# Optimization experiments

Measured on AMD Instinct MI355X. Metric: run time of the kernel, lower is better.

## Reference

```python
import jax, jax.numpy as jnp
import numpy as np

N = 50000      # nodes
E = 800000     # edges
IN = 128       # in_dim
EMB = 32       # emb_dim
ED = 8         # edge_dim
L = 4          # num_layers
B = 64         # num graphs in batch
OUT = 10       # out_dim
EPS = 1e-5


def setup_inputs() -> dict:
    key = jax.random.key(0)
    ks = jax.random.split(key, 16)
    f32 = jnp.float32
    def nrm(k, shape, scale):
        return jax.random.normal(k, shape, dtype=f32) * scale
    inp = {}
    inp['x'] = nrm(ks[0], (N, IN), 1.0)
    inp['edge_index'] = jax.random.randint(ks[1], (2, E), 0, N)
    inp['edge_attr'] = nrm(ks[2], (E, ED), 1.0)
    inp['batch'] = jnp.sort(jax.random.randint(ks[3], (N,), 0, B))
    # lin_in
    inp['lin_in_w'] = nrm(ks[4], (IN, EMB), 0.05)
    inp['lin_in_b'] = jnp.zeros((EMB,), f32)
    # per-layer message MLP: Linear(2e+ed->e), BN, ReLU, Linear(e->e), BN, ReLU
    inp['msg_w1'] = nrm(ks[5], (L, 2 * EMB + ED, EMB), 0.1)
    inp['msg_b1'] = jnp.zeros((L, EMB), f32)
    inp['msg_g1'] = jnp.ones((L, EMB), f32)
    inp['msg_be1'] = jnp.zeros((L, EMB), f32)
    inp['msg_w2'] = nrm(ks[6], (L, EMB, EMB), 0.1)
    inp['msg_b2'] = jnp.zeros((L, EMB), f32)
    inp['msg_g2'] = jnp.ones((L, EMB), f32)
    inp['msg_be2'] = jnp.zeros((L, EMB), f32)
    # per-layer update MLP: Linear(2e->e), BN, ReLU, Linear(e->e), BN, ReLU
    inp['upd_w1'] = nrm(ks[7], (L, 2 * EMB, EMB), 0.1)
    inp['upd_b1'] = jnp.zeros((L, EMB), f32)
    inp['upd_g1'] = jnp.ones((L, EMB), f32)
    inp['upd_be1'] = jnp.zeros((L, EMB), f32)
    inp['upd_w2'] = nrm(ks[8], (L, EMB, EMB), 0.1)
    inp['upd_b2'] = jnp.zeros((L, EMB), f32)
    inp['upd_g2'] = jnp.ones((L, EMB), f32)
    inp['upd_be2'] = jnp.zeros((L, EMB), f32)
    # lin_pred
    inp['pred_w'] = nrm(ks[9], (EMB, OUT), 0.1)
    inp['pred_b'] = jnp.zeros((OUT,), f32)
    return inp


def _bn(x, g, b):
    # BatchNorm1d in training mode: batch stats over dim 0 (biased variance)
    mu = jnp.mean(x, axis=0)
    var = jnp.mean(jnp.square(x - mu), axis=0)
    return (x - mu) * jax.lax.rsqrt(var + EPS) * g + b


def reference(x, edge_attr, lin_in_w, lin_in_b,
              msg_w1, msg_b1, msg_g1, msg_be1, msg_w2, msg_b2, msg_g2, msg_be2,
              upd_w1, upd_b1, upd_g1, upd_be1, upd_w2, upd_b2, upd_g2, upd_be2,
              pred_w, pred_b, edge_index, batch):
    src = edge_index[0]  # h_j source nodes
    dst = edge_index[1]  # h_i target nodes (aggregation index)
    h = x @ lin_in_w + lin_in_b  # [N, EMB]
    for i in range(L):
        # message: gather + concat + MLP(BN,ReLU)x2 over edges
        msg_in = jnp.concatenate([h[dst], h[src], edge_attr], axis=-1)  # [E, 2e+ed]
        m = jax.nn.relu(_bn(msg_in @ msg_w1[i] + msg_b1[i], msg_g1[i], msg_be1[i]))
        m = jax.nn.relu(_bn(m @ msg_w2[i] + msg_b2[i], msg_g2[i], msg_be2[i]))
        # aggregate: scatter-add by destination
        aggr = jax.ops.segment_sum(m, dst, num_segments=N)  # [N, EMB]
        # update: concat + MLP(BN,ReLU)x2
        u = jnp.concatenate([h, aggr], axis=-1)  # [N, 2e]
        u = jax.nn.relu(_bn(u @ upd_w1[i] + upd_b1[i], upd_g1[i], upd_be1[i]))
        u = jax.nn.relu(_bn(u @ upd_w2[i] + upd_b2[i], upd_g2[i], upd_be2[i]))
        h = u + h  # residual in MPNNModel.get_embeddings
    # global mean pool
    sums = jax.ops.segment_sum(h, batch, num_segments=B)
    counts = jax.ops.segment_sum(jnp.ones((N,), h.dtype), batch, num_segments=B)
    h_graph = sums / jnp.maximum(counts, 1.0)[:, None]
    return h_graph @ pred_w + pred_b  # [B, OUT]
```

## Files before the change

kernel.cpp:

```cpp
#include <hip/hip_runtime.h>
#include <cstddef>

#define N_NODES 50000
#define N_EDGES 800000
#define IN_DIM  128
#define EMB     32
#define ED      8
#define NLAYERS 4
#define NB      64
#define OUTD    10
#define EPS_BN  1e-5f

#define EDGE_GRID 3125
#define NODE_GRID 196
#define NODE4_GRID 782
#define AU_GRID   6250
#define MSG1_EPT  2
#define MSG1_GRID 1563
#define NT16      50000
#define NTILE_N   3125
#define LIN_GRID  782
#define MSG2_TPW  16
#define MSG2_GRID 782

#define SREP 4

typedef short bf16x8 __attribute__((ext_vector_type(8)));
typedef float f32x4  __attribute__((ext_vector_type(4)));


__device__ __forceinline__ unsigned short f2bf(float x) {
  union { float f; unsigned u; } v; v.f = x;
  unsigned b = v.u + 0x7FFFu + ((v.u >> 16) & 1u);
  return (unsigned short)(b >> 16);
}
__device__ __forceinline__ float bf2f(unsigned short s) {
  union { unsigned u; float f; } v; v.u = ((unsigned)s) << 16;
  return v.f;
}

__device__ __forceinline__ void coef_from_stats(const float* __restrict__ stats_stage,
                                                const float* __restrict__ g,
                                                const float* __restrict__ be,
                                                float inv_count, float* __restrict__ cf) {
  if (threadIdx.x < EMB) {
    const int c = threadIdx.x;
    float s = 0.f, ss = 0.f;
#pragma unroll
    for (int r = 0; r < SREP; ++r) {
      s  += stats_stage[r*64 + c];
      ss += stats_stage[r*64 + EMB + c];
    }
    const float mu  = s * inv_count;
    const float var = ss * inv_count - mu*mu;
    const float a = g[c] * rsqrtf(var + EPS_BN);
    cf[c] = a;
    cf[EMB + c] = fmaf(-mu, a, be[c]);
  }
  __syncthreads();
}

__device__ __forceinline__ void block_stats_atomic(const float ts[EMB], const float tss[EMB],
                                                   float* __restrict__ stats_stage) {
  __shared__ float sred[256];
  const int lane = threadIdx.x & 63;
  const int wid  = threadIdx.x >> 6;
#pragma unroll
  for (int c = 0; c < EMB; ++c) {
    float a = ts[c];
    float q = tss[c];
#pragma unroll
    for (int o = 32; o > 0; o >>= 1) {
      a += __shfl_down(a, o, 64);
      q += __shfl_down(q, o, 64);
    }
    if (lane == 0) { sred[wid*64 + c] = a; sred[wid*64 + EMB + c] = q; }
  }
  __syncthreads();
  if (threadIdx.x < 64) {
    const float v = sred[threadIdx.x] + sred[64 + threadIdx.x] +
                    sred[128 + threadIdx.x] + sred[192 + threadIdx.x];
    atomicAdd(stats_stage + ((blockIdx.x & (SREP-1)) << 6) + threadIdx.x, v);
  }
}

__device__ __forceinline__ void wave_stats_atomic(float ts[8], float tss[8],
                                                  float* __restrict__ lds_s,
                                                  float* __restrict__ lds_q,
                                                  float* __restrict__ stats_stage) {
  const int lane = threadIdx.x & 63;
  const int wv   = threadIdx.x >> 6;
#pragma unroll
  for (int j = 0; j < 8; ++j) {
    float a = ts[j], b = tss[j];
#pragma unroll
    for (int o = 32; o > 0; o >>= 1) {
      a += __shfl_down(a, o, 64);
      b += __shfl_down(b, o, 64);
    }
    ts[j] = a; tss[j] = b;
  }
  if (lane == 0) {
#pragma unroll
    for (int j = 0; j < 8; ++j) {
      lds_s[wv*8 + j] = ts[j];
      lds_q[wv*8 + j] = tss[j];
    }
  }
  __syncthreads();
  if (threadIdx.x < 64) {
    const float v = (threadIdx.x < 32) ? lds_s[threadIdx.x] : lds_q[threadIdx.x - 32];
    atomicAdd(stats_stage + ((blockIdx.x & (SREP-1)) << 6) + threadIdx.x, v);
  }
}

#define HSTRIDE 40

__global__ __launch_bounds__(256) void k_lin_in_pq(
    const float* __restrict__ x, const float* __restrict__ w, const float* __restrict__ b,
    const float* __restrict__ w1, const float* __restrict__ b1, const int* __restrict__ ei,
    float* __restrict__ h, unsigned short* __restrict__ p, unsigned short* __restrict__ q,
    int* __restrict__ cnt)
{
  __shared__ __align__(16) unsigned short lds_hb[4][16*HSTRIDE];
  __shared__ __align__(16) unsigned short lds_pq[4][16*HSTRIDE];
  const int lane = threadIdx.x & 63;
  const int wv   = threadIdx.x >> 6;
  const int n0i  = lane & 15;
  const int quad = lane >> 4;

  const int tile = blockIdx.x*4 + wv;
  if (tile < NTILE_N) {
    const int r0 = tile*16;
    bf16x8 BwL[4], BwH[4];
#pragma unroll
    for (int kb = 0; kb < 4; ++kb) {
#pragma unroll
      for (int j = 0; j < 8; ++j) {
        const int k = kb*32 + quad*8 + j;
        BwL[kb][j] = (short)f2bf(w[k*EMB + n0i]);
        BwH[kb][j] = (short)f2bf(w[k*EMB + 16 + n0i]);
      }
    }
    f32x4 accL = {0.f,0.f,0.f,0.f};
    f32x4 accH = {0.f,0.f,0.f,0.f};
#pragma unroll
    for (int kb = 0; kb < 4; ++kb) {
      const float4 xa = *(const float4*)(x + (size_t)(r0 + n0i)*IN_DIM + kb*32 + quad*8);
      const float4 xb = *(const float4*)(x + (size_t)(r0 + n0i)*IN_DIM + kb*32 + quad*8 + 4);
      bf16x8 A;
      A[0] = (short)f2bf(xa.x); A[1] = (short)f2bf(xa.y);
      A[2] = (short)f2bf(xa.z); A[3] = (short)f2bf(xa.w);
      A[4] = (short)f2bf(xb.x); A[5] = (short)f2bf(xb.y);
      A[6] = (short)f2bf(xb.z); A[7] = (short)f2bf(xb.w);
      accL = __builtin_amdgcn_mfma_f32_16x16x32_bf16(A, BwL[kb], accL, 0, 0, 0);
      accH = __builtin_amdgcn_mfma_f32_16x16x32_bf16(A, BwH[kb], accH, 0, 0, 0);
    }
    const float bL = b[n0i], bH = b[16 + n0i];
#pragma unroll
    for (int r = 0; r < 4; ++r) {
      const int row = quad*4 + r;
      const float vL = accL[r] + bL;
      const float vH = accH[r] + bH;
      h[(size_t)(r0 + row)*EMB + n0i]      = vL;
      h[(size_t)(r0 + row)*EMB + 16 + n0i] = vH;
      lds_hb[wv][row*HSTRIDE + n0i]      = f2bf(vL);
      lds_hb[wv][row*HSTRIDE + 16 + n0i] = f2bf(vH);
    }
    bf16x8 A2;
#pragma unroll
    for (int j = 0; j < 8; ++j)
      A2[j] = (short)lds_hb[wv][n0i*HSTRIDE + quad*8 + j];
    bf16x8 BpL, BpH, BqL, BqH;
#pragma unroll
    for (int j = 0; j < 8; ++j) {
      const int k = quad*8 + j;
      BpL[j] = (short)f2bf(w1[k*EMB + n0i]);
      BpH[j] = (short)f2bf(w1[k*EMB + 16 + n0i]);
      BqL[j] = (short)f2bf(w1[(EMB + k)*EMB + n0i]);
      BqH[j] = (short)f2bf(w1[(EMB + k)*EMB + 16 + n0i]);
    }
    const f32x4 z4 = {0.f,0.f,0.f,0.f};
    f32x4 pL = __builtin_amdgcn_mfma_f32_16x16x32_bf16(A2, BpL, z4, 0, 0, 0);
    f32x4 pH = __builtin_amdgcn_mfma_f32_16x16x32_bf16(A2, BpH, z4, 0, 0, 0);
    f32x4 qL = __builtin_amdgcn_mfma_f32_16x16x32_bf16(A2, BqL, z4, 0, 0, 0);
    f32x4 qH = __builtin_amdgcn_mfma_f32_16x16x32_bf16(A2, BqH, z4, 0, 0, 0);
    const float b1L = b1[n0i], b1H = b1[16 + n0i];
#pragma unroll
    for (int r = 0; r < 4; ++r) {
      const int row = quad*4 + r;
      lds_pq[wv][row*HSTRIDE + n0i]      = f2bf(pL[r] + b1L);
      lds_pq[wv][row*HSTRIDE + 16 + n0i] = f2bf(pH[r] + b1H);
    }
    {
      const int row2 = lane >> 2;
      const int c8   = (lane & 3)*8;
      const uint4 ov = *(const uint4*)&lds_pq[wv][row2*HSTRIDE + c8];
      *(uint4*)(p + (size_t)(r0 + row2)*EMB + c8) = ov;
    }
#pragma unroll
    for (int r = 0; r < 4; ++r) {
      const int row = quad*4 + r;
      lds_pq[wv][row*HSTRIDE + n0i]      = f2bf(qL[r]);
      lds_pq[wv][row*HSTRIDE + 16 + n0i] = f2bf(qH[r]);
    }
    {
      const int row2 = lane >> 2;
      const int c8   = (lane & 3)*8;
      const uint4 ov = *(const uint4*)&lds_pq[wv][row2*HSTRIDE + c8];
      *(uint4*)(q + (size_t)(r0 + row2)*EMB + c8) = ov;
    }
  }
  for (int e = blockIdx.x*256 + threadIdx.x; e < N_EDGES; e += gridDim.x*256)
    atomicAdd(&cnt[ei[N_EDGES + e]], 1);
}

__global__ __launch_bounds__(256) void k_scan_a(const int* __restrict__ cnt,
                                                int* __restrict__ row_ptr, int* __restrict__ bsum) {
  __shared__ int s[256];
  const int gid = blockIdx.x*256 + threadIdx.x;
  const int v = (gid < N_NODES) ? cnt[gid] : 0;
  s[threadIdx.x] = v;
  __syncthreads();
  for (int o = 1; o < 256; o <<= 1) {
    const int t = (threadIdx.x >= o) ? s[threadIdx.x - o] : 0;
    __syncthreads();
    s[threadIdx.x] += t;
    __syncthreads();
  }
  if (gid < N_NODES) row_ptr[gid] = s[threadIdx.x] - v;
  if (threadIdx.x == 255) bsum[blockIdx.x] = s[255];
}

__global__ __launch_bounds__(256) void k_scan_bc(int* __restrict__ row_ptr,
                                                 const int* __restrict__ bsum) {
  __shared__ int s[256];
  const int t = threadIdx.x;
  const int v = (t < NODE_GRID) ? bsum[t] : 0;
  s[t] = v;
  __syncthreads();
  for (int o = 1; o < 256; o <<= 1) {
    const int tt = (t >= o) ? s[t - o] : 0;
    __syncthreads();
    s[t] += tt;
    __syncthreads();
  }
  const int off = (blockIdx.x == 0) ? 0 : s[blockIdx.x - 1];
  const int gid = blockIdx.x*256 + t;
  if (gid < N_NODES) row_ptr[gid] += off;
  if (blockIdx.x == 0 && t == 0) row_ptr[N_NODES] = N_EDGES;
}

__global__ __launch_bounds__(256) void k_place(const int* __restrict__ ei,
                                               const int* __restrict__ row_ptr,
                                               int* __restrict__ cnt2, int* __restrict__ perm) {
  const int e = blockIdx.x*256 + threadIdx.x;
  const int d = ei[N_EDGES + e];
  const int pos = row_ptr[d] + atomicAdd(&cnt2[d], 1);
  perm[pos] = e;
}

__global__ __launch_bounds__(256) void k_permute(
    const int* __restrict__ perm, const int* __restrict__ ei, const float* __restrict__ ea,
    int* __restrict__ src_perm, int* __restrict__ dst_perm, unsigned short* __restrict__ ea_perm)
{
  const int i = blockIdx.x*256 + threadIdx.x;
  const int e = perm[i];
  src_perm[i] = ei[e];
  dst_perm[i] = ei[N_EDGES + e];
  const float4 v0 = ((const float4*)(ea + (size_t)e*ED))[0];
  const float4 v1 = ((const float4*)(ea + (size_t)e*ED))[1];
  const float ev[8] = {v0.x, v0.y, v0.z, v0.w, v1.x, v1.y, v1.z, v1.w};
  unsigned u[4];
#pragma unroll
  for (int j = 0; j < 4; ++j)
    u[j] = (unsigned)f2bf(ev[2*j]) | ((unsigned)f2bf(ev[2*j+1]) << 16);
  uint4 o; o.x = u[0]; o.y = u[1]; o.z = u[2]; o.w = u[3];
  *(uint4*)(ea_perm + (size_t)i*ED) = o;
}


__global__ __launch_bounds__(256) void k_msg1(
    const unsigned short* __restrict__ pb, const unsigned short* __restrict__ qb,
    const int* __restrict__ src_perm, const int* __restrict__ dst_perm,
    const unsigned short* __restrict__ ea_perm,
    const float* __restrict__ w1b,
    unsigned short* __restrict__ y, float* __restrict__ stats)
{
  float ts[EMB], tss[EMB];
#pragma unroll
  for (int c = 0; c < EMB; ++c) { ts[c] = 0.f; tss[c] = 0.f; }
  const int base = blockIdx.x*(256*MSG1_EPT) + threadIdx.x;
  for (int it = 0; it < MSG1_EPT; ++it) {
    const int i = base + it*256;
    if (i >= N_EDGES) break;
    const int dst = dst_perm[i];
    const int src = src_perm[i];
    float acc[EMB];
    const uint4* pd = (const uint4*)(pb + (size_t)dst*EMB);
    const uint4* qs = (const uint4*)(qb + (size_t)src*EMB);
#pragma unroll
    for (int j4 = 0; j4 < 4; ++j4) {
      const uint4 a = pd[j4];
      const uint4 b = qs[j4];
      const unsigned ua[4] = {a.x, a.y, a.z, a.w};
      const unsigned ub[4] = {b.x, b.y, b.z, b.w};
#pragma unroll
      for (int t = 0; t < 4; ++t) {
        acc[j4*8 + 2*t]   = bf2f((unsigned short)(ua[t] & 0xFFFFu)) +
                            bf2f((unsigned short)(ub[t] & 0xFFFFu));
        acc[j4*8 + 2*t+1] = bf2f((unsigned short)(ua[t] >> 16)) +
                            bf2f((unsigned short)(ub[t] >> 16));
      }
    }
    const uint4 eraw = *(const uint4*)(ea_perm + (size_t)i*ED);
    const unsigned ue[4] = {eraw.x, eraw.y, eraw.z, eraw.w};
    float ev[8];
#pragma unroll
    for (int t = 0; t < 4; ++t) {
      ev[2*t]   = bf2f((unsigned short)(ue[t] & 0xFFFFu));
      ev[2*t+1] = bf2f((unsigned short)(ue[t] >> 16));
    }
#pragma unroll
    for (int k = 0; k < 8; ++k) {
      const float* wk = w1b + k*EMB;
#pragma unroll
      for (int c = 0; c < EMB; ++c) acc[c] = fmaf(ev[k], wk[c], acc[c]);
    }
    unsigned short us[EMB];
#pragma unroll
    for (int c = 0; c < EMB; ++c) us[c] = f2bf(acc[c]);
    unsigned u[16];
#pragma unroll
    for (int j = 0; j < 16; ++j)
      u[j] = (unsigned)us[2*j] | ((unsigned)us[2*j+1] << 16);
    uint4* dp = (uint4*)(y + (size_t)i*EMB);
#pragma unroll
    for (int j = 0; j < 4; ++j) {
      uint4 o; o.x = u[4*j]; o.y = u[4*j+1]; o.z = u[4*j+2]; o.w = u[4*j+3];
      dp[j] = o;
    }
#pragma unroll
    for (int c = 0; c < EMB; ++c) {
      const float v = bf2f(us[c]);
      ts[c] += v;
      tss[c] = fmaf(v, v, tss[c]);
    }
  }
  block_stats_atomic(ts, tss, stats);
}

__global__ __launch_bounds__(256) void k_msg2(
    unsigned short* __restrict__ y,
    const float* __restrict__ stats1, const float* __restrict__ g1, const float* __restrict__ be1,
    const float* __restrict__ w2, const float* __restrict__ b2,
    float* __restrict__ stats2)
{
  __shared__ __align__(16) unsigned short lds_t[4][16*32];
  __shared__ float lds_s[4][32], lds_q[4][32];
  __shared__ float cf[64];

  coef_from_stats(stats1, g1, be1, 1.0f/(float)N_EDGES, cf);

  const int lane = threadIdx.x & 63;
  const int wid  = threadIdx.x >> 6;
  const int n0 = lane & 15;
  const int kb = lane >> 4;

  bf16x8 Blo, Bhi;
#pragma unroll
  for (int j = 0; j < 8; ++j) {
    Blo[j] = (short)f2bf(w2[(kb*8 + j)*EMB + n0]);
    Bhi[j] = (short)f2bf(w2[(kb*8 + j)*EMB + 16 + n0]);
  }
  float a1[8], c1[8];
#pragma unroll
  for (int j = 0; j < 8; ++j) {
    a1[j] = cf[kb*8 + j];
    c1[j] = cf[EMB + kb*8 + j];
  }
  const float b2c0 = b2[n0], b2c1 = b2[16 + n0];

  float ts[8], tss[8];
#pragma unroll
  for (int j = 0; j < 8; ++j) { ts[j] = 0.f; tss[j] = 0.f; }

  const int tile0 = blockIdx.x * (MSG2_TPW*4);
  for (int t = 0; t < MSG2_TPW; ++t) {
    const int tile = tile0 + t*4 + wid;
    if (tile >= NT16) break;
    const size_t e0 = (size_t)tile * 16;

    const uint4 araw = *(const uint4*)(y + (e0 + n0)*EMB + kb*8);
    unsigned int ua[4] = {araw.x, araw.y, araw.z, araw.w};
    bf16x8 A;
#pragma unroll
    for (int j = 0; j < 4; ++j) {
      float v0 = bf2f((unsigned short)(ua[j] & 0xFFFFu));
      float v1 = bf2f((unsigned short)(ua[j] >> 16));
      v0 = fmaxf(fmaf(a1[2*j],   v0, c1[2*j]),   0.f);
      v1 = fmaxf(fmaf(a1[2*j+1], v1, c1[2*j+1]), 0.f);
      A[2*j]   = (short)f2bf(v0);
      A[2*j+1] = (short)f2bf(v1);
    }

    f32x4 acc0 = {0.f, 0.f, 0.f, 0.f};
    f32x4 acc1 = {0.f, 0.f, 0.f, 0.f};
    acc0 = __builtin_amdgcn_mfma_f32_16x16x32_bf16(A, Blo, acc0, 0, 0, 0);
    acc1 = __builtin_amdgcn_mfma_f32_16x16x32_bf16(A, Bhi, acc1, 0, 0, 0);

#pragma unroll
    for (int r = 0; r < 4; ++r) {
      const int row = kb*4 + r;
      lds_t[wid][row*32 + n0]      = f2bf(acc0[r] + b2c0);
      lds_t[wid][row*32 + 16 + n0] = f2bf(acc1[r] + b2c1);
    }
    const uint4 orow = *(const uint4*)&lds_t[wid][(lane>>2)*32 + (lane&3)*8];
    *(uint4*)(y + (e0 + (lane>>2))*EMB + (lane&3)*8) = orow;

    unsigned int uo[4] = {orow.x, orow.y, orow.z, orow.w};
#pragma unroll
    for (int j = 0; j < 4; ++j) {
      const float v0 = bf2f((unsigned short)(uo[j] & 0xFFFFu));
      const float v1 = bf2f((unsigned short)(uo[j] >> 16));
      ts[2*j]   += v0;  tss[2*j]   = fmaf(v0, v0, tss[2*j]);
      ts[2*j+1] += v1;  tss[2*j+1] = fmaf(v1, v1, tss[2*j+1]);
    }
  }

#pragma unroll
  for (int j = 0; j < 8; ++j) {
    float s = ts[j], qq = tss[j];
#pragma unroll
    for (int o = 4; o < 64; o <<= 1) {
      s  += __shfl_xor(s, o, 64);
      qq += __shfl_xor(qq, o, 64);
    }
    ts[j] = s; tss[j] = qq;
  }
  if (lane < 4) {
#pragma unroll
    for (int j = 0; j < 8; ++j) {
      lds_s[wid][lane*8 + j] = ts[j];
      lds_q[wid][lane*8 + j] = tss[j];
    }
  }
  __syncthreads();
  if (threadIdx.x < 64) {
    const int c = threadIdx.x & 31;
    const int kind = threadIdx.x >> 5;
    float v = 0.f;
#pragma unroll
    for (int wq = 0; wq < 4; ++wq)
      v += kind ? lds_q[wq][c] : lds_s[wq][c];
    atomicAdd(stats2 + ((blockIdx.x & (SREP-1)) << 6) + kind*32 + c, v);
  }
}

__global__ __launch_bounds__(256) void k_aggr_upd1(
    const unsigned short* __restrict__ y, const int* __restrict__ row_ptr,
    const float* __restrict__ h,
    const float* __restrict__ stats1, const float* __restrict__ g2, const float* __restrict__ be2,
    const float* __restrict__ uw1, const float* __restrict__ ub1,
    float* __restrict__ z, float* __restrict__ stats2)
{
  __shared__ float cf[64];
  __shared__ float lh[8][32];
  __shared__ float la[8][32];
  __shared__ float rs[4][32], rq[4][32];
  coef_from_stats(stats1, g2, be2, 1.0f/(float)N_EDGES, cf);

  const int g = threadIdx.x >> 5;
  const int l = threadIdx.x & 31;
  const int n = blockIdx.x*8 + g;

  lh[g][l] = h[(size_t)n*EMB + l];

  const int rof = l >> 4;
  const int cp  = l & 15;
  const float a0 = cf[2*cp],     b0 = cf[EMB + 2*cp];
  const float a1 = cf[2*cp + 1], b1 = cf[EMB + 2*cp + 1];
  const int lo = row_ptr[n], hi = row_ptr[n+1];
  float s0 = 0.f, s1 = 0.f;
  for (int i = lo + rof; i < hi; i += 2) {
    const unsigned u = *(const unsigned*)(y + (size_t)i*EMB + 2*cp);
    const float v0 = bf2f((unsigned short)(u & 0xFFFFu));
    const float v1 = bf2f((unsigned short)(u >> 16));
    s0 += fmaxf(fmaf(a0, v0, b0), 0.f);
    s1 += fmaxf(fmaf(a1, v1, b1), 0.f);
  }
  s0 += __shfl_xor(s0, 16, 64);
  s1 += __shfl_xor(s1, 16, 64);
  if (rof == 0) { la[g][2*cp] = s0; la[g][2*cp + 1] = s1; }
  __syncthreads();

  float acc = ub1[l];
#pragma unroll
  for (int k = 0; k < EMB; ++k) acc = fmaf(lh[g][k], uw1[k*EMB + l], acc);
#pragma unroll
  for (int k = 0; k < EMB; ++k) acc = fmaf(la[g][k], uw1[(EMB + k)*EMB + l], acc);
  z[(size_t)n*EMB + l] = acc;

  const float sq = acc*acc;
  const float a2 = acc + __shfl_down(acc, 32, 64);
  const float q2 = sq  + __shfl_down(sq,  32, 64);
  const int wv = threadIdx.x >> 6;
  if ((threadIdx.x & 63) < 32) { rs[wv][l] = a2; rq[wv][l] = q2; }
  __syncthreads();
  if (threadIdx.x < 64) {
    const int c = threadIdx.x & 31;
    const int kind = threadIdx.x >> 5;
    float v = 0.f;
#pragma unroll
    for (int wq = 0; wq < 4; ++wq)
      v += kind ? rq[wq][c] : rs[wq][c];
    atomicAdd(stats2 + ((blockIdx.x & (SREP-1)) << 6) + kind*32 + c, v);
  }
}

__global__ __launch_bounds__(256) void k_upd2(
    float* __restrict__ z,
    const float* __restrict__ stats1, const float* __restrict__ g1, const float* __restrict__ be1,
    const float* __restrict__ w, const float* __restrict__ b,
    float* __restrict__ stats2)
{
  __shared__ float cf[64];
  __shared__ float lds_s[32], lds_q[32];
  coef_from_stats(stats1, g1, be1, 1.0f/(float)N_NODES, cf);

  const int lane = threadIdx.x & 63;
  const int wv   = threadIdx.x >> 6;
  const int n  = blockIdx.x*64 + lane;
  const int c0 = wv*8;
  float acc[8];
#pragma unroll
  for (int j = 0; j < 8; ++j) acc[j] = 0.f;
  if (n < N_NODES) {
#pragma unroll
    for (int j = 0; j < 8; ++j) acc[j] = b[c0 + j];
    const float4* zp = (const float4*)(z + (size_t)n*EMB);
#pragma unroll
    for (int k4 = 0; k4 < 8; ++k4) {
      const float4 v = zp[k4];
      const float mv[4] = {v.x, v.y, v.z, v.w};
#pragma unroll
      for (int t = 0; t < 4; ++t) {
        const int k = 4*k4 + t;
        const float m = fmaxf(fmaf(cf[k], mv[t], cf[EMB + k]), 0.f);
        const float* wk = w + k*EMB + c0;
#pragma unroll
        for (int j = 0; j < 8; ++j) acc[j] = fmaf(m, wk[j], acc[j]);
      }
    }
  }
  float ts[8], tss[8];
#pragma unroll
  for (int j = 0; j < 8; ++j) { ts[j] = acc[j]; tss[j] = acc[j]*acc[j]; }
  wave_stats_atomic(ts, tss, lds_s, lds_q, stats2);
  if (n < N_NODES) {
    float4 o0, o1;
    o0.x = acc[0]; o0.y = acc[1]; o0.z = acc[2]; o0.w = acc[3];
    o1.x = acc[4]; o1.y = acc[5]; o1.z = acc[6]; o1.w = acc[7];
    *(float4*)(z + (size_t)n*EMB + c0)     = o0;
    *(float4*)(z + (size_t)n*EMB + c0 + 4) = o1;
  }
}

__global__ __launch_bounds__(256) void k_resid_pq(
    float* __restrict__ h, const float* __restrict__ z,
    const float* __restrict__ stats, const float* __restrict__ g, const float* __restrict__ be,
    const float* __restrict__ w1_next, const float* __restrict__ b1_next,
    unsigned short* __restrict__ p, unsigned short* __restrict__ q)
{
  __shared__ float cf[64];
  __shared__ float lds_h[64][33];
  coef_from_stats(stats, g, be, 1.0f/(float)N_NODES, cf);

  const int lane = threadIdx.x & 63;
  const int wv   = threadIdx.x >> 6;
  const int n  = blockIdx.x*64 + lane;
  const int c0 = wv*8;
  if (n < N_NODES) {
    const float4* zp = (const float4*)(z + (size_t)n*EMB + c0);
    float4* hp = (float4*)(h + (size_t)n*EMB + c0);
    float hn[8];
    const float4 z0 = zp[0], z1 = zp[1];
    const float4 h0 = hp[0], h1 = hp[1];
    const float zv[8] = {z0.x, z0.y, z0.z, z0.w, z1.x, z1.y, z1.z, z1.w};
    const float hv[8] = {h0.x, h0.y, h0.z, h0.w, h1.x, h1.y, h1.z, h1.w};
#pragma unroll
    for (int j = 0; j < 8; ++j) {
      const int k = c0 + j;
      hn[j] = hv[j] + fmaxf(fmaf(cf[k], zv[j], cf[EMB + k]), 0.f);
      lds_h[lane][k] = hn[j];
    }
    float4 o0, o1;
    o0.x = hn[0]; o0.y = hn[1]; o0.z = hn[2]; o0.w = hn[3];
    o1.x = hn[4]; o1.y = hn[5]; o1.z = hn[6]; o1.w = hn[7];
    hp[0] = o0; hp[1] = o1;
  }
  __syncthreads();
  if (n < N_NODES && w1_next) {
    float ap[8], aq[8];
#pragma unroll
    for (int j = 0; j < 8; ++j) { ap[j] = b1_next[c0 + j]; aq[j] = 0.f; }
#pragma unroll
    for (int k = 0; k < EMB; ++k) {
      const float hvv = lds_h[lane][k];
      const float* wp = w1_next + k*EMB + c0;
      const float* wq = w1_next + (EMB + k)*EMB + c0;
#pragma unroll
      for (int j = 0; j < 8; ++j) ap[j] = fmaf(hvv, wp[j], ap[j]);
#pragma unroll
      for (int j = 0; j < 8; ++j) aq[j] = fmaf(hvv, wq[j], aq[j]);
    }
    unsigned up[4], uq[4];
#pragma unroll
    for (int j = 0; j < 4; ++j) {
      up[j] = (unsigned)f2bf(ap[2*j]) | ((unsigned)f2bf(ap[2*j+1]) << 16);
      uq[j] = (unsigned)f2bf(aq[2*j]) | ((unsigned)f2bf(aq[2*j+1]) << 16);
    }
    uint4 op; op.x = up[0]; op.y = up[1]; op.z = up[2]; op.w = up[3];
    uint4 oq; oq.x = uq[0]; oq.y = uq[1]; oq.z = uq[2]; oq.w = uq[3];
    *(uint4*)(p + (size_t)n*EMB + c0) = op;
    *(uint4*)(q + (size_t)n*EMB + c0) = oq;
  }
}

__global__ void k_pool(const float* __restrict__ h, const int* __restrict__ batch,
                       const float* __restrict__ pw, const float* __restrict__ pb,
                       float* __restrict__ out)
{
  __shared__ float sred[256];
  __shared__ float hg[EMB];
  const int b = blockIdx.x;
  int lo = 0, hi = N_NODES;
  while (lo < hi) { int m = (lo + hi) >> 1; if (batch[m] < b) lo = m + 1; else hi = m; }
  const int start = lo;
  hi = N_NODES;
  while (lo < hi) { int m = (lo + hi) >> 1; if (batch[m] < b + 1) lo = m + 1; else hi = m; }
  const int end = lo;

  const int c = threadIdx.x & (EMB-1);
  const int r = threadIdx.x >> 5;
  float s = 0.f;
  for (int n = start + r; n < end; n += 8) s += h[(size_t)n*EMB + c];
  sred[threadIdx.x] = s;
  __syncthreads();
  if (threadIdx.x < EMB) {
    float tot = 0.f;
#pragma unroll
    for (int r2 = 0; r2 < 8; ++r2) tot += sred[r2*EMB + threadIdx.x];
    const float cnt = (float)(end - start);
    hg[threadIdx.x] = tot / fmaxf(cnt, 1.f);
  }
  __syncthreads();
  if (threadIdx.x < OUTD) {
    float acc = pb[threadIdx.x];
#pragma unroll
    for (int cc = 0; cc < EMB; ++cc) acc = fmaf(hg[cc], pw[cc*OUTD + threadIdx.x], acc);
    out[b*OUTD + threadIdx.x] = acc;
  }
}


extern "C" void kernel_launch(void* const* d_in, const int* in_sizes, int n_in,
                              void* d_out, int out_size, void* d_ws, size_t ws_size,
                              hipStream_t stream) {
  const float* x        = (const float*)d_in[0];
  const int*   ei       = (const int*)  d_in[1];
  const float* ea       = (const float*)d_in[2];
  const int*   batch    = (const int*)  d_in[3];
  const float* lin_in_w = (const float*)d_in[4];
  const float* lin_in_b = (const float*)d_in[5];
  const float* msg_w1   = (const float*)d_in[6];
  const float* msg_b1   = (const float*)d_in[7];
  const float* msg_g1   = (const float*)d_in[8];
  const float* msg_be1  = (const float*)d_in[9];
  const float* msg_w2   = (const float*)d_in[10];
  const float* msg_b2   = (const float*)d_in[11];
  const float* msg_g2   = (const float*)d_in[12];
  const float* msg_be2  = (const float*)d_in[13];
  const float* upd_w1   = (const float*)d_in[14];
  const float* upd_b1   = (const float*)d_in[15];
  const float* upd_g1   = (const float*)d_in[16];
  const float* upd_be1  = (const float*)d_in[17];
  const float* upd_w2   = (const float*)d_in[18];
  const float* upd_b2   = (const float*)d_in[19];
  const float* upd_g2   = (const float*)d_in[20];
  const float* upd_be2  = (const float*)d_in[21];
  const float* pred_w   = (const float*)d_in[22];
  const float* pred_b   = (const float*)d_in[23];
  float* out = (float*)d_out;

  char* wsb = (char*)d_ws;
  unsigned short* y  = (unsigned short*)wsb;
  unsigned short* eap= (unsigned short*)(wsb + (size_t)N_EDGES*EMB*2);
  unsigned short* p  = eap + (size_t)N_EDGES*ED;
  unsigned short* q  = p + (size_t)N_NODES*EMB;
  float* h       = (float*)(q + (size_t)N_NODES*EMB);
  float* z       = h + (size_t)N_NODES*EMB;
  float* stats   = z + (size_t)N_NODES*EMB;
  int*   cnt     = (int*)(stats + 16*SREP*64);
  int*   cnt2    = cnt + N_NODES;
  int*   row_ptr = cnt2 + N_NODES;
  int*   bsum    = row_ptr + N_NODES + 1;
  int*   perm    = bsum + 256;
  int*   src_perm= perm + N_EDGES;
  int*   dst_perm= src_perm + N_EDGES;
  const size_t need = ((size_t)((char*)(dst_perm + N_EDGES) - wsb));
  if (ws_size < need) return;

  hipMemsetAsync(stats, 0, (16*SREP*64 + 2*N_NODES)*sizeof(float), stream);

  k_lin_in_pq<<<LIN_GRID, 256, 0, stream>>>(x, lin_in_w, lin_in_b, msg_w1, msg_b1, ei,
                                            h, p, q, cnt);
  k_scan_a<<<NODE_GRID, 256, 0, stream>>>(cnt, row_ptr, bsum);
  k_scan_bc<<<NODE_GRID, 256, 0, stream>>>(row_ptr, bsum);
  k_place<<<EDGE_GRID, 256, 0, stream>>>(ei, row_ptr, cnt2, perm);
  k_permute<<<EDGE_GRID, 256, 0, stream>>>(perm, ei, ea, src_perm, dst_perm, eap);

  for (int l = 0; l < NLAYERS; ++l) {
    const int st = l*4;
    const float* w1  = msg_w1 + (size_t)l*(2*EMB+ED)*EMB;
    const float* w1b = w1 + (size_t)2*EMB*EMB;
    const float* w2  = msg_w2 + (size_t)l*EMB*EMB;
    const float* uw1 = upd_w1 + (size_t)l*(2*EMB)*EMB;
    const float* uw2 = upd_w2 + (size_t)l*EMB*EMB;
    const float* w1_next = (l+1 < NLAYERS) ? msg_w1 + (size_t)(l+1)*(2*EMB+ED)*EMB : nullptr;
    const float* b1_next = (l+1 < NLAYERS) ? msg_b1 + (size_t)(l+1)*EMB : nullptr;

    k_msg1<<<MSG1_GRID, 256, 0, stream>>>(p, q, src_perm, dst_perm, eap,
                                          w1b, y, stats + (size_t)st*SREP*64);
    k_msg2<<<MSG2_GRID, 256, 0, stream>>>(y, stats + (size_t)st*SREP*64,
                                          msg_g1 + l*EMB, msg_be1 + l*EMB,
                                          w2, msg_b2 + l*EMB, stats + (size_t)(st+1)*SREP*64);
    k_aggr_upd1<<<AU_GRID, 256, 0, stream>>>(y, row_ptr, h,
                                             stats + (size_t)(st+1)*SREP*64,
                                             msg_g2 + l*EMB, msg_be2 + l*EMB,
                                             uw1, upd_b1 + l*EMB,
                                             z, stats + (size_t)(st+2)*SREP*64);
    k_upd2<<<NODE4_GRID, 256, 0, stream>>>(z, stats + (size_t)(st+2)*SREP*64,
                                           upd_g1 + l*EMB, upd_be1 + l*EMB,
                                           uw2, upd_b2 + l*EMB, stats + (size_t)(st+3)*SREP*64);
    k_resid_pq<<<NODE4_GRID, 256, 0, stream>>>(h, z, stats + (size_t)(st+3)*SREP*64,
                                               upd_g2 + l*EMB, upd_be2 + l*EMB,
                                               w1_next, b1_next, p, q);
  }

  k_pool<<<NB, 256, 0, stream>>>(h, batch, pred_w, pred_b, out);
}
```

Measured before the change: 904.3 us.

## Recompute first message linear layer instead of storing intermediate edge activations

The first message kernel now only accumulates BatchNorm statistics and no longer writes the per-edge pre-BN activations. A fused kernel recomputes the gather plus edge-attr linear layer, applies BN1 and ReLU, runs the second linear layer on MFMA through LDS, and writes the output and its statistics. This drops one full E×32 bf16 write and one read per layer, paid for by a second round of gathers from p/q and repeated edge-attr FMAs. Stats are now taken from fp32 values rather than bf16-rounded ones, a small numerical change.

```diff
diff --git a/kernel.cpp b/kernel.cpp
--- a/kernel.cpp
+++ b/kernel.cpp
@@ -17,12 +17,11 @@
 #define AU_GRID   6250
 #define MSG1_EPT  2
 #define MSG1_GRID 1563
-#define NT16      50000
+#define NCHUNK    12500
+#define MSG12_CPW 4
+#define MSG12_GRID 782
 #define NTILE_N   3125
 #define LIN_GRID  782
-#define MSG2_TPW  16
-#define MSG2_GRID 782
-
 #define SREP 4
 
 typedef short bf16x8 __attribute__((ext_vector_type(8)));
@@ -111,6 +110,42 @@
   if (threadIdx.x < 64) {
     const float v = (threadIdx.x < 32) ? lds_s[threadIdx.x] : lds_q[threadIdx.x - 32];
     atomicAdd(stats_stage + ((blockIdx.x & (SREP-1)) << 6) + threadIdx.x, v);
+  }
+}
+
+__device__ __forceinline__ void y1_compute(float acc[EMB],
+    const unsigned short* __restrict__ pb, const unsigned short* __restrict__ qb,
+    int dst, int src, const unsigned short* __restrict__ ea_perm, int i,
+    const float* __restrict__ w1b) {
+  const uint4* pd = (const uint4*)(pb + (size_t)dst*EMB);
+  const uint4* qs = (const uint4*)(qb + (size_t)src*EMB);
+#pragma unroll
+  for (int j4 = 0; j4 < 4; ++j4) {
+    const uint4 a = pd[j4];
+    const uint4 b = qs[j4];
+    const unsigned ua[4] = {a.x, a.y, a.z, a.w};
+    const unsigned ub[4] = {b.x, b.y, b.z, b.w};
+#pragma unroll
+    for (int t = 0; t < 4; ++t) {
+      acc[j4*8 + 2*t]   = bf2f((unsigned short)(ua[t] & 0xFFFFu)) +
+                          bf2f((unsigned short)(ub[t] & 0xFFFFu));
+      acc[j4*8 + 2*t+1] = bf2f((unsigned short)(ua[t] >> 16)) +
+                          bf2f((unsigned short)(ub[t] >> 16));
+    }
+  }
+  const uint4 eraw = *(const uint4*)(ea_perm + (size_t)i*ED);
+  const unsigned ue[4] = {eraw.x, eraw.y, eraw.z, eraw.w};
+  float ev[8];
+#pragma unroll
+  for (int t = 0; t < 4; ++t) {
+    ev[2*t]   = bf2f((unsigned short)(ue[t] & 0xFFFFu));
+    ev[2*t+1] = bf2f((unsigned short)(ue[t] >> 16));
+  }
+#pragma unroll
+  for (int k = 0; k < 8; ++k) {
+    const float* wk = w1b + k*EMB;
+#pragma unroll
+    for (int c = 0; c < EMB; ++c) acc[c] = fmaf(ev[k], wk[c], acc[c]);
   }
 }
 
@@ -280,12 +315,11 @@
 }
 
 
-__global__ __launch_bounds__(256) void k_msg1(
+__global__ __launch_bounds__(256) void k_msg1_stats(
     const unsigned short* __restrict__ pb, const unsigned short* __restrict__ qb,
     const int* __restrict__ src_perm, const int* __restrict__ dst_perm,
     const unsigned short* __restrict__ ea_perm,
-    const float* __restrict__ w1b,
-    unsigned short* __restrict__ y, float* __restrict__ stats)
+    const float* __restrict__ w1b, float* __restrict__ stats)
 {
   float ts[EMB], tss[EMB];
 #pragma unroll
@@ -294,137 +328,113 @@
   for (int it = 0; it < MSG1_EPT; ++it) {
     const int i = base + it*256;
     if (i >= N_EDGES) break;
-    const int dst = dst_perm[i];
-    const int src = src_perm[i];
     float acc[EMB];
-    const uint4* pd = (const uint4*)(pb + (size_t)dst*EMB);
-    const uint4* qs = (const uint4*)(qb + (size_t)src*EMB);
-#pragma unroll
-    for (int j4 = 0; j4 < 4; ++j4) {
-      const uint4 a = pd[j4];
-      const uint4 b = qs[j4];
-      const unsigned ua[4] = {a.x, a.y, a.z, a.w};
-      const unsigned ub[4] = {b.x, b.y, b.z, b.w};
-#pragma unroll
-      for (int t = 0; t < 4; ++t) {
-        acc[j4*8 + 2*t]   = bf2f((unsigned short)(ua[t] & 0xFFFFu)) +
-                            bf2f((unsigned short)(ub[t] & 0xFFFFu));
-        acc[j4*8 + 2*t+1] = bf2f((unsigned short)(ua[t] >> 16)) +
-                            bf2f((unsigned short)(ub[t] >> 16));
-      }
-    }
-    const uint4 eraw = *(const uint4*)(ea_perm + (size_t)i*ED);
-    const unsigned ue[4] = {eraw.x, eraw.y, eraw.z, eraw.w};
-    float ev[8];
-#pragma unroll
-    for (int t = 0; t < 4; ++t) {
-      ev[2*t]   = bf2f((unsigned short)(ue[t] & 0xFFFFu));
-      ev[2*t+1] = bf2f((unsigned short)(ue[t] >> 16));
-    }
-#pragma unroll
-    for (int k = 0; k < 8; ++k) {
-      const float* wk = w1b + k*EMB;
-#pragma unroll
-      for (int c = 0; c < EMB; ++c) acc[c] = fmaf(ev[k], wk[c], acc[c]);
-    }
-    unsigned short us[EMB];
-#pragma unroll
-    for (int c = 0; c < EMB; ++c) us[c] = f2bf(acc[c]);
-    unsigned u[16];
-#pragma unroll
-    for (int j = 0; j < 16; ++j)
-      u[j] = (unsigned)us[2*j] | ((unsigned)us[2*j+1] << 16);
-    uint4* dp = (uint4*)(y + (size_t)i*EMB);
-#pragma unroll
-    for (int j = 0; j < 4; ++j) {
-      uint4 o; o.x = u[4*j]; o.y = u[4*j+1]; o.z = u[4*j+2]; o.w = u[4*j+3];
-      dp[j] = o;
-    }
+    y1_compute(acc, pb, qb, dst_perm[i], src_perm[i], ea_perm, i, w1b);
 #pragma unroll
     for (int c = 0; c < EMB; ++c) {
-      const float v = bf2f(us[c]);
-      ts[c] += v;
-      tss[c] = fmaf(v, v, tss[c]);
+      ts[c] += acc[c];
+      tss[c] = fmaf(acc[c], acc[c], tss[c]);
     }
   }
   block_stats_atomic(ts, tss, stats);
 }
 
-__global__ __launch_bounds__(256) void k_msg2(
-    unsigned short* __restrict__ y,
+#define MSTRIDE 40
+__global__ __launch_bounds__(256) void k_msg12(
+    const unsigned short* __restrict__ pb, const unsigned short* __restrict__ qb,
+    const int* __restrict__ src_perm, const int* __restrict__ dst_perm,
+    const unsigned short* __restrict__ ea_perm,
+    const float* __restrict__ w1b,
     const float* __restrict__ stats1, const float* __restrict__ g1, const float* __restrict__ be1,
     const float* __restrict__ w2, const float* __restrict__ b2,
-    float* __restrict__ stats2)
+    unsigned short* __restrict__ y, float* __restrict__ stats2)
 {
-  __shared__ __align__(16) unsigned short lds_t[4][16*32];
+  __shared__ __align__(16) unsigned short lds_a[4][64*MSTRIDE];
   __shared__ float lds_s[4][32], lds_q[4][32];
   __shared__ float cf[64];
 
   coef_from_stats(stats1, g1, be1, 1.0f/(float)N_EDGES, cf);
 
   const int lane = threadIdx.x & 63;
-  const int wid  = threadIdx.x >> 6;
-  const int n0 = lane & 15;
-  const int kb = lane >> 4;
+  const int wv   = threadIdx.x >> 6;
+  const int n0i  = lane & 15;
+  const int kb   = lane >> 4;
 
   bf16x8 Blo, Bhi;
 #pragma unroll
   for (int j = 0; j < 8; ++j) {
-    Blo[j] = (short)f2bf(w2[(kb*8 + j)*EMB + n0]);
-    Bhi[j] = (short)f2bf(w2[(kb*8 + j)*EMB + 16 + n0]);
-  }
-  float a1[8], c1[8];
-#pragma unroll
-  for (int j = 0; j < 8; ++j) {
-    a1[j] = cf[kb*8 + j];
-    c1[j] = cf[EMB + kb*8 + j];
-  }
-  const float b2c0 = b2[n0], b2c1 = b2[16 + n0];
+    Blo[j] = (short)f2bf(w2[(kb*8 + j)*EMB + n0i]);
+    Bhi[j] = (short)f2bf(w2[(kb*8 + j)*EMB + 16 + n0i]);
+  }
+  const float b2c0 = b2[n0i], b2c1 = b2[16 + n0i];
+  float a1[EMB], c1[EMB];
+#pragma unroll
+  for (int c = 0; c < EMB; ++c) { a1[c] = cf[c]; c1[c] = cf[EMB + c]; }
 
   float ts[8], tss[8];
 #pragma unroll
   for (int j = 0; j < 8; ++j) { ts[j] = 0.f; tss[j] = 0.f; }
 
-  const int tile0 = blockIdx.x * (MSG2_TPW*4);
-  for (int t = 0; t < MSG2_TPW; ++t) {
-    const int tile = tile0 + t*4 + wid;
-    if (tile >= NT16) break;
-    const size_t e0 = (size_t)tile * 16;
-
-    const uint4 araw = *(const uint4*)(y + (e0 + n0)*EMB + kb*8);
-    unsigned int ua[4] = {araw.x, araw.y, araw.z, araw.w};
-    bf16x8 A;
+  const int chunk0 = (blockIdx.x*4 + wv)*MSG12_CPW;
+  for (int cix = 0; cix < MSG12_CPW; ++cix) {
+    const int chunk = chunk0 + cix;
+    if (chunk >= NCHUNK) break;
+    const size_t e0 = (size_t)chunk*64;
+    const int i = (int)e0 + lane;
+
+    {
+      float acc[EMB];
+      y1_compute(acc, pb, qb, dst_perm[i], src_perm[i], ea_perm, i, w1b);
+      unsigned u[16];
+#pragma unroll
+      for (int j = 0; j < 16; ++j) {
+        const float v0 = fmaxf(fmaf(a1[2*j],   acc[2*j],   c1[2*j]),   0.f);
+        const float v1 = fmaxf(fmaf(a1[2*j+1], acc[2*j+1], c1[2*j+1]), 0.f);
+        u[j] = (unsigned)f2bf(v0) | ((unsigned)f2bf(v1) << 16);
+      }
+      uint4* row = (uint4*)&lds_a[wv][lane*MSTRIDE];
+#pragma unroll
+      for (int j = 0; j < 4; ++j) {
+        uint4 o; o.x = u[4*j]; o.y = u[4*j+1]; o.z = u[4*j+2]; o.w = u[4*j+3];
+        row[j] = o;
+      }
+    }
+#pragma unroll
+    for (int t = 0; t < 4; ++t) {
+      const uint4 araw = *(const uint4*)&lds_a[wv][(16*t + n0i)*MSTRIDE + kb*8];
+      bf16x8 A;
+      const unsigned ua[4] = {araw.x, araw.y, araw.z, araw.w};
+#pragma unroll
+      for (int j = 0; j < 4; ++j) {
+        A[2*j]   = (short)(ua[j] & 0xFFFFu);
+        A[2*j+1] = (short)(ua[j] >> 16);
+      }
+      f32x4 acc0 = {0.f, 0.f, 0.f, 0.f};
+      f32x4 acc1 = {0.f, 0.f, 0.f, 0.f};
+      acc0 = __builtin_amdgcn_mfma_f32_16x16x32_bf16(A, Blo, acc0, 0, 0, 0);
+      acc1 = __builtin_amdgcn_mfma_f32_16x16x32_bf16(A, Bhi, acc1, 0, 0, 0);
+#pragma unroll
+      for (int r = 0; r < 4; ++r) {
+        const int row = 16*t + kb*4 + r;
+        lds_a[wv][row*MSTRIDE + n0i]      = f2bf(acc0[r] + b2c0);
+        lds_a[wv][row*MSTRIDE + 16 + n0i] = f2bf(acc1[r] + b2c1);
+      }
+    }
 #pragma unroll
     for (int j = 0; j < 4; ++j) {
-      float v0 = bf2f((unsigned short)(ua[j] & 0xFFFFu));
-      float v1 = bf2f((unsigned short)(ua[j] >> 16));
-      v0 = fmaxf(fmaf(a1[2*j],   v0, c1[2*j]),   0.f);
-      v1 = fmaxf(fmaf(a1[2*j+1], v1, c1[2*j+1]), 0.f);
-      A[2*j]   = (short)f2bf(v0);
-      A[2*j+1] = (short)f2bf(v1);
-    }
-
-    f32x4 acc0 = {0.f, 0.f, 0.f, 0.f};
-    f32x4 acc1 = {0.f, 0.f, 0.f, 0.f};
-    acc0 = __builtin_amdgcn_mfma_f32_16x16x32_bf16(A, Blo, acc0, 0, 0, 0);
-    acc1 = __builtin_amdgcn_mfma_f32_16x16x32_bf16(A, Bhi, acc1, 0, 0, 0);
-
-#pragma unroll
-    for (int r = 0; r < 4; ++r) {
-      const int row = kb*4 + r;
-      lds_t[wid][row*32 + n0]      = f2bf(acc0[r] + b2c0);
-      lds_t[wid][row*32 + 16 + n0] = f2bf(acc1[r] + b2c1);
-    }
-    const uint4 orow = *(const uint4*)&lds_t[wid][(lane>>2)*32 + (lane&3)*8];
-    *(uint4*)(y + (e0 + (lane>>2))*EMB + (lane&3)*8) = orow;
-
-    unsigned int uo[4] = {orow.x, orow.y, orow.z, orow.w};
-#pragma unroll
-    for (int j = 0; j < 4; ++j) {
-      const float v0 = bf2f((unsigned short)(uo[j] & 0xFFFFu));
-      const float v1 = bf2f((unsigned short)(uo[j] >> 16));
-      ts[2*j]   += v0;  tss[2*j]   = fmaf(v0, v0, tss[2*j]);
-      ts[2*j+1] += v1;  tss[2*j+1] = fmaf(v1, v1, tss[2*j+1]);
+      const int c64 = lane + 64*j;
+      const int row = c64 >> 2;
+      const int c8  = (c64 & 3)*8;
+      const uint4 ov = *(const uint4*)&lds_a[wv][row*MSTRIDE + c8];
+      *(uint4*)(y + (e0 + row)*EMB + c8) = ov;
+      const unsigned uo[4] = {ov.x, ov.y, ov.z, ov.w};
+#pragma unroll
+      for (int jj = 0; jj < 4; ++jj) {
+        const float v0 = bf2f((unsigned short)(uo[jj] & 0xFFFFu));
+        const float v1 = bf2f((unsigned short)(uo[jj] >> 16));
+        ts[2*jj]   += v0;  tss[2*jj]   = fmaf(v0, v0, tss[2*jj]);
+        ts[2*jj+1] += v1;  tss[2*jj+1] = fmaf(v1, v1, tss[2*jj+1]);
+      }
     }
   }
 
@@ -441,8 +451,8 @@
   if (lane < 4) {
 #pragma unroll
     for (int j = 0; j < 8; ++j) {
-      lds_s[wid][lane*8 + j] = ts[j];
-      lds_q[wid][lane*8 + j] = tss[j];
+      lds_s[wv][lane*8 + j] = ts[j];
+      lds_q[wv][lane*8 + j] = tss[j];
     }
   }
   __syncthreads();
@@ -730,11 +740,13 @@
     const float* w1_next = (l+1 < NLAYERS) ? msg_w1 + (size_t)(l+1)*(2*EMB+ED)*EMB : nullptr;
     const float* b1_next = (l+1 < NLAYERS) ? msg_b1 + (size_t)(l+1)*EMB : nullptr;
 
-    k_msg1<<<MSG1_GRID, 256, 0, stream>>>(p, q, src_perm, dst_perm, eap,
-                                          w1b, y, stats + (size_t)st*SREP*64);
-    k_msg2<<<MSG2_GRID, 256, 0, stream>>>(y, stats + (size_t)st*SREP*64,
-                                          msg_g1 + l*EMB, msg_be1 + l*EMB,
-                                          w2, msg_b2 + l*EMB, stats + (size_t)(st+1)*SREP*64);
+    k_msg1_stats<<<MSG1_GRID, 256, 0, stream>>>(p, q, src_perm, dst_perm, eap,
+                                                w1b, stats + (size_t)st*SREP*64);
+    k_msg12<<<MSG12_GRID, 256, 0, stream>>>(p, q, src_perm, dst_perm, eap, w1b,
+                                            stats + (size_t)st*SREP*64,
+                                            msg_g1 + l*EMB, msg_be1 + l*EMB,
+                                            w2, msg_b2 + l*EMB,
+                                            y, stats + (size_t)(st+1)*SREP*64);
     k_aggr_upd1<<<AU_GRID, 256, 0, stream>>>(y, row_ptr, h,
                                              stats + (size_t)(st+1)*SREP*64,
                                              msg_g2 + l*EMB, msg_be2 + l*EMB,
```

After: 906.9 us. Within noise of the previous version (+0.3%).
